# Kernel optimization log

Hardware: AMD Instinct MI355X
Metric: run time of the kernel (lower is better)

Reference implementation:

```python
import jax, jax.numpy as jnp
import numpy as np

D_MODEL = 1024
N_HEADS = 16
B, T = 16, 512


def setup_inputs() -> dict:
    key = jax.random.key(0)
    ks = jax.random.split(key, 5)
    s = 0.02
    return {
        "x": jax.random.normal(ks[0], (B, T, D_MODEL), dtype=jnp.float32),
        "w_qkv": jax.random.normal(ks[1], (D_MODEL, 3 * D_MODEL), dtype=jnp.float32) * s,
        "b_qkv": jax.random.normal(ks[2], (3 * D_MODEL,), dtype=jnp.float32) * s,
        "w_o": jax.random.normal(ks[3], (D_MODEL, D_MODEL), dtype=jnp.float32) * s,
        "b_o": jax.random.normal(ks[4], (D_MODEL,), dtype=jnp.float32) * s,
    }


def reference(x, w_qkv, b_qkv, w_o, b_o):
    Bx, Tx, C = x.shape
    H = N_HEADS
    hd = C // H
    qkv = x @ w_qkv + b_qkv                      # [B,T,3C]
    qkv = qkv.reshape(Bx, Tx, 3, H, hd).transpose(2, 0, 3, 1, 4)  # [3,B,H,T,hd]
    q, k, v = qkv[0], qkv[1], qkv[2]
    # NOTE: original scales by sqrt(C) = sqrt(d_model), not sqrt(head_dim)
    att = jnp.einsum("bhqd,bhkd->bhqk", q, k) / jnp.sqrt(jnp.float32(C))
    causal = jnp.tril(jnp.ones((Tx, Tx), dtype=bool))
    att = jnp.where(causal, att, -jnp.inf)
    att = jax.nn.softmax(att, axis=-1)
    y = jnp.einsum("bhqk,bhkd->bhqd", att, v)    # [B,H,T,hd]
    y = y.transpose(0, 2, 1, 3).reshape(Bx, Tx, C)
    return y @ w_o + b_o
```

## Files before the change

### kernel.cpp

```cpp
#include <hip/hip_runtime.h>
#include <cstddef>


#define B_  16
#define T_  512
#define C_  1024
#define H_  16
#define HD_ 64

typedef __bf16 bf16x8 __attribute__((ext_vector_type(8)));
typedef float  f32x4  __attribute__((ext_vector_type(4)));

__device__ __forceinline__ void gload16(const void* g, void* lds_dst) {
  __builtin_amdgcn_global_load_lds(
      (const __attribute__((address_space(1))) unsigned int*)g,
      (__attribute__((address_space(3))) unsigned int*)lds_dst, 16, 0, 0);
}

__global__ void cvt_kernel(const float* __restrict__ in, __bf16* __restrict__ out, int n) {
  int i = (blockIdx.x * 256 + threadIdx.x) * 8;
  if (i >= n) return;
  float4 f0 = *(const float4*)&in[i];
  float4 f1 = *(const float4*)&in[i + 4];
  bf16x8 o;
  o[0] = (__bf16)f0.x; o[1] = (__bf16)f0.y; o[2] = (__bf16)f0.z; o[3] = (__bf16)f0.w;
  o[4] = (__bf16)f1.x; o[5] = (__bf16)f1.y; o[6] = (__bf16)f1.z; o[7] = (__bf16)f1.w;
  *(bf16x8*)&out[i] = o;
}

__global__ void tconv_kernel(const float* __restrict__ w, __bf16* __restrict__ wt,
                             int K, int N) {
  __shared__ float tile[32][33];
  int tx = threadIdx.x, ty = threadIdx.y;
  int n0 = blockIdx.x * 32, k0 = blockIdx.y * 32;
  #pragma unroll
  for (int i = 0; i < 4; ++i) {
    int r = ty + i * 8;
    tile[r][tx] = w[(size_t)(k0 + r) * N + n0 + tx];
  }
  __syncthreads();
  #pragma unroll
  for (int i = 0; i < 4; ++i) {
    int r = ty + i * 8;
    wt[(size_t)(n0 + r) * K + k0 + tx] = (__bf16)tile[tx][r];
  }
}

__global__ void vtr_kernel(const __bf16* __restrict__ v, __bf16* __restrict__ vt) {
  __shared__ __bf16 tile[64][68];
  const int tid = threadIdx.x;
  const int bh = blockIdx.x, tc = blockIdx.y;
  const size_t base = (size_t)bh * T_ * HD_;
  #pragma unroll
  for (int p = 0; p < 2; ++p) {
    int t8 = p * 256 + tid;
    int r = t8 >> 3, col = (t8 & 7) * 8;
    *(bf16x8*)&tile[r][col] =
        *(const bf16x8*)&v[base + (size_t)(tc * 64 + r) * HD_ + col];
  }
  __syncthreads();
  #pragma unroll
  for (int p = 0; p < 2; ++p) {
    int t8 = p * 256 + tid;
    int d = t8 >> 3, tt = (t8 & 7) * 8;
    bf16x8 o;
    #pragma unroll
    for (int i = 0; i < 8; ++i) o[i] = tile[tt + i][d];
    *(bf16x8*)&vt[base + (size_t)d * T_ + tc * 64 + tt] = o;
  }
}

__global__ __launch_bounds__(512, 2) void gemm192_kernel(
    const __bf16* __restrict__ A, const __bf16* __restrict__ BT,
    const float* __restrict__ bias, int K, int NBn,
    __bf16* __restrict__ oq, __bf16* __restrict__ okk, __bf16* __restrict__ ov)
{
  extern __shared__ __align__(16) char lds[];
  const int tid = threadIdx.x, lane = tid & 63, wid = tid >> 6;
  const int wm = wid >> 2, wn = wid & 3;
  const int lr = lane & 15, lg = lane >> 4;

  const int cpx = gridDim.x >> 3;
  const int id = (blockIdx.x & 7) * cpx + (blockIdx.x >> 3);
  const int m0 = (id / NBn) * 256, n0 = (id % NBn) * 192;

  const int r8  = wid * 8 + (lane >> 3);
  const int csw = ((lane & 7) ^ (lane >> 3)) * 8;

  auto stageA = [&](const __bf16* g, char* dst) {
    #pragma unroll
    for (int i = 0; i < 4; ++i)
      gload16(g + (size_t)(i * 64 + r8) * K + csw, dst + i * 8192 + wid * 1024);
  };
  auto stageB = [&](const __bf16* g, char* dst) {
    #pragma unroll
    for (int i = 0; i < 3; ++i)
      gload16(g + (size_t)(i * 64 + r8) * K + csw, dst + i * 8192 + wid * 1024);
  };

  auto rdA = [&](bf16x8* d, const char* Ab) {
    #pragma unroll
    for (int mf = 0; mf < 8; ++mf) {
      const char* rp = Ab + (wm * 128 + mf * 16 + lr) * 128;
      #pragma unroll
      for (int ks = 0; ks < 2; ++ks)
        d[mf * 2 + ks] = *(const bf16x8*)(rp + (((ks << 2) + lg) ^ (lr & 7)) * 16);
    }
  };
  auto rdB = [&](bf16x8* d, const char* Bb) {
    #pragma unroll
    for (int nf = 0; nf < 3; ++nf) {
      const char* rp = Bb + (wn * 48 + nf * 16 + lr) * 128;
      #pragma unroll
      for (int ks = 0; ks < 2; ++ks)
        d[nf * 2 + ks] = *(const bf16x8*)(rp + (((ks << 2) + lg) ^ (lr & 7)) * 16);
    }
  };

  f32x4 acc[8][3] = {};

  auto mm = [&](int mh, const bf16x8* av, const bf16x8* bv) {
    __builtin_amdgcn_s_setprio(1);
    #pragma unroll
    for (int mf = 0; mf < 4; ++mf)
      #pragma unroll
      for (int nf = 0; nf < 3; ++nf)
        #pragma unroll
        for (int ks = 0; ks < 2; ++ks)
          acc[mh * 4 + mf][nf] = __builtin_amdgcn_mfma_f32_16x16x32_bf16(
              av[(mh * 4 + mf) * 2 + ks], bv[nf * 2 + ks], acc[mh * 4 + mf][nf],
              0, 0, 0);
    __builtin_amdgcn_s_setprio(0);
  };

  const int nt = K >> 6;
  const __bf16* gA = A  + (size_t)m0 * K;
  const __bf16* gB = BT + (size_t)n0 * K;
  char* const Ab0 = lds;
  char* const Bb0 = lds + 65536;

  stageA(gA, Ab0);
  stageB(gB, Bb0);
  stageA(gA + 64, Ab0 + 32768);

  bf16x8 a[16], b[6];

  for (int t = 0; t < nt; ++t) {
    const int p = t & 1;
    char* Ab = Ab0 + p * 32768;
    char* Bb = Bb0 + p * 24576;
    char* Bn = Bb0 + (p ^ 1) * 24576;

    if (t + 1 < nt) { asm volatile("s_waitcnt vmcnt(4)\ns_barrier" ::: "memory"); }
    else            { asm volatile("s_waitcnt vmcnt(0)\ns_barrier" ::: "memory"); }
    rdB(b, Bb);
    rdA(a, Ab);
    if (t + 1 < nt) stageB(gB + (size_t)(t + 1) * 64, Bn);
    mm(0, a, b);
    asm volatile("s_barrier" ::: "memory");

    if (t + 2 < nt) stageA(gA + (size_t)(t + 2) * 64, Ab);
    mm(1, a, b);
    asm volatile("s_barrier" ::: "memory");
  }

  #pragma unroll
  for (int nf = 0; nf < 3; ++nf) {
    int n = n0 + wn * 48 + nf * 16 + lr;
    float bv = bias[n];
    int which = n >> 10;
    __bf16* dst = (which == 0) ? oq : (which == 1) ? okk : ov;
    int h = (n >> 6) & 15, d = n & 63;
    #pragma unroll
    for (int mf = 0; mf < 8; ++mf)
      #pragma unroll
      for (int j = 0; j < 4; ++j) {
        int m = m0 + wm * 128 + mf * 16 + lg * 4 + j;
        int bb = m >> 9, tt = m & 511;
        dst[(size_t)((bb * H_ + h) * T_ + tt) * HD_ + d] =
            (__bf16)(acc[mf][nf][j] + bv);
      }
  }
}

__global__ __launch_bounds__(512, 2) void gemm128_kernel(
    const __bf16* __restrict__ A, const __bf16* __restrict__ BT,
    const float* __restrict__ bias, int K, int NBn, int N,
    float* __restrict__ out32)
{
  extern __shared__ __align__(16) char lds[];
  const int tid = threadIdx.x, lane = tid & 63, wid = tid >> 6;
  const int wm = wid >> 2, wn = wid & 3;
  const int lr = lane & 15, lg = lane >> 4;

  const int cpx = gridDim.x >> 3;
  const int id = (blockIdx.x & 7) * cpx + (blockIdx.x >> 3);
  const int m0 = (id / NBn) * 128, n0 = (id % NBn) * 256;

  const int r8  = wid * 8 + (lane >> 3);
  const int csw = ((lane & 7) ^ (lane >> 3)) * 8;

  auto stageA = [&](const __bf16* g, char* dst) {
    #pragma unroll
    for (int i = 0; i < 2; ++i)
      gload16(g + (size_t)(i * 64 + r8) * K + csw, dst + i * 8192 + wid * 1024);
  };
  auto stageB = [&](const __bf16* g, char* dst) {
    #pragma unroll
    for (int i = 0; i < 4; ++i)
      gload16(g + (size_t)(i * 64 + r8) * K + csw, dst + i * 8192 + wid * 1024);
  };

  auto rdA = [&](bf16x8* d, const char* Ab) {
    #pragma unroll
    for (int mf = 0; mf < 4; ++mf) {
      const char* rp = Ab + (wm * 64 + mf * 16 + lr) * 128;
      #pragma unroll
      for (int ks = 0; ks < 2; ++ks)
        d[mf * 2 + ks] = *(const bf16x8*)(rp + (((ks << 2) + lg) ^ (lr & 7)) * 16);
    }
  };
  auto rdB = [&](bf16x8* d, const char* Bb, int nh) {
    #pragma unroll
    for (int nfl = 0; nfl < 2; ++nfl) {
      const char* rp = Bb + (wn * 64 + (nh * 2 + nfl) * 16 + lr) * 128;
      #pragma unroll
      for (int ks = 0; ks < 2; ++ks)
        d[nfl * 2 + ks] = *(const bf16x8*)(rp + (((ks << 2) + lg) ^ (lr & 7)) * 16);
    }
  };

  f32x4 acc[4][4] = {};

  auto mm = [&](const bf16x8* av, const bf16x8* bv, int nh) {
    __builtin_amdgcn_s_setprio(1);
    #pragma unroll
    for (int mf = 0; mf < 4; ++mf)
      #pragma unroll
      for (int nfl = 0; nfl < 2; ++nfl)
        #pragma unroll
        for (int ks = 0; ks < 2; ++ks)
          acc[mf][nh * 2 + nfl] = __builtin_amdgcn_mfma_f32_16x16x32_bf16(
              av[mf * 2 + ks], bv[nfl * 2 + ks], acc[mf][nh * 2 + nfl], 0, 0, 0);
    __builtin_amdgcn_s_setprio(0);
  };

  const int nt = K >> 6;
  const __bf16* gA = A  + (size_t)m0 * K;
  const __bf16* gB = BT + (size_t)n0 * K;
  char* const Ab0 = lds;
  char* const Bb0 = lds + 32768;

  stageB(gB, Bb0);
  stageA(gA, Ab0);
  stageB(gB + 64, Bb0 + 32768);
  stageA(gA + 64, Ab0 + 16384);

  bf16x8 a[8], b0[4], b1[4];

  for (int t = 0; t < nt; ++t) {
    char* Ab = Ab0 + (t & 1) * 16384;
    char* Bb = Bb0 + (t % 3) * 32768;

    if (t + 1 < nt) { asm volatile("s_waitcnt vmcnt(6)\ns_barrier" ::: "memory"); }
    else            { asm volatile("s_waitcnt vmcnt(0)\ns_barrier" ::: "memory"); }
    rdA(a, Ab);
    rdB(b0, Bb, 0);
    if (t + 2 < nt) stageB(gB + (size_t)(t + 2) * 64, Bb0 + ((t + 2) % 3) * 32768);
    mm(a, b0, 0);
    asm volatile("s_barrier" ::: "memory");

    rdB(b1, Bb, 1);
    if (t + 2 < nt) stageA(gA + (size_t)(t + 2) * 64, Ab);
    mm(a, b1, 1);
    asm volatile("s_barrier" ::: "memory");
  }

  #pragma unroll
  for (int nf = 0; nf < 4; ++nf) {
    int n = n0 + wn * 64 + nf * 16 + lr;
    float bv = bias[n];
    #pragma unroll
    for (int mf = 0; mf < 4; ++mf)
      #pragma unroll
      for (int j = 0; j < 4; ++j) {
        int m = m0 + wm * 64 + mf * 16 + lg * 4 + j;
        out32[(size_t)m * N + n] = acc[mf][nf][j] + bv;
      }
  }
}

__global__ __launch_bounds__(256, 2) void attn_kernel(
    const __bf16* __restrict__ qb, const __bf16* __restrict__ kb,
    const __bf16* __restrict__ vtb, __bf16* __restrict__ y)
{
  __shared__ __attribute__((aligned(16))) __bf16 Ks[64][72];
  __shared__ __attribute__((aligned(16))) __bf16 Vt[64][72];
  __shared__ __attribute__((aligned(16))) __bf16 Ps[4][16][72];

  const int tid = threadIdx.x, lane = tid & 63, w = tid >> 6;
  const int lr = lane & 15, lg = lane >> 4;
  const int bh = blockIdx.x, qt = blockIdx.y;
  const size_t base = (size_t)bh * T_ * HD_;
  const int q0 = qt * 64 + w * 16;
  const float SCALE = 0.03125f;
  const float L2E = 1.44269504088896f;

  const int r_  = tid >> 3;
  const int c8_ = (tid & 7) * 8;

  bf16x8 qf[2];
  #pragma unroll
  for (int s = 0; s < 2; ++s)
    qf[s] = *(const bf16x8*)&qb[base + (size_t)(q0 + lr) * HD_ + s * 32 + lg * 8];

  f32x4 acc[4] = {};
  float mrun[4] = { -__builtin_inff(), -__builtin_inff(),
                    -__builtin_inff(), -__builtin_inff() };
  float lrun[4] = { 0.f, 0.f, 0.f, 0.f };

  bf16x8 kk[2], vv[2], kk2[2], vv2[2];
  #pragma unroll
  for (int p = 0; p < 2; ++p) {
    int rr = p * 32 + r_;
    kk[p] = *(const bf16x8*)&kb[base + (size_t)rr * HD_ + c8_];
    vv[p] = *(const bf16x8*)&vtb[base + (size_t)rr * T_ + c8_];
  }

  for (int c = 0; c <= qt; ++c) {
    #pragma unroll
    for (int p = 0; p < 2; ++p) {
      int rr = p * 32 + r_;
      *(bf16x8*)&Ks[rr][c8_] = kk[p];
      *(bf16x8*)&Vt[rr][c8_] = vv[p];
    }
    __syncthreads();

    if (c < qt) {
      #pragma unroll
      for (int p = 0; p < 2; ++p) {
        int rr = p * 32 + r_;
        kk2[p] = *(const bf16x8*)&kb[base + (size_t)(c + 1) * 64 * HD_ + (size_t)rr * HD_ + c8_];
        vv2[p] = *(const bf16x8*)&vtb[base + (size_t)rr * T_ + (c + 1) * 64 + c8_];
      }
    }

    f32x4 sc[4] = {};
    #pragma unroll
    for (int s = 0; s < 2; ++s) {
      #pragma unroll
      for (int cc = 0; cc < 4; ++cc) {
        bf16x8 kf = *(const bf16x8*)&Ks[cc * 16 + lr][s * 32 + lg * 8];
        sc[cc] = __builtin_amdgcn_mfma_f32_16x16x32_bf16(qf[s], kf, sc[cc], 0, 0, 0);
      }
    }

    #pragma unroll
    for (int cc = 0; cc < 4; ++cc)
      #pragma unroll
      for (int j = 0; j < 4; ++j) {
        float v = sc[cc][j] * SCALE;
        if (c == qt) {
          int kv = c * 64 + cc * 16 + lr;
          int qr = q0 + lg * 4 + j;
          if (kv > qr) v = -__builtin_inff();
        }
        sc[cc][j] = v;
      }

    float mx[4];
    #pragma unroll
    for (int j = 0; j < 4; ++j)
      mx[j] = fmaxf(fmaxf(sc[0][j], sc[1][j]), fmaxf(sc[2][j], sc[3][j]));
    #pragma unroll
    for (int msk = 1; msk <= 8; msk <<= 1)
      #pragma unroll
      for (int j = 0; j < 4; ++j)
        mx[j] = fmaxf(mx[j], __shfl_xor(mx[j], msk, 64));
    float corr[4];
    #pragma unroll
    for (int j = 0; j < 4; ++j) {
      float nm = fmaxf(mrun[j], mx[j]);
      corr[j] = exp2f((mrun[j] - nm) * L2E);
      mrun[j] = nm;
    }
    #pragma unroll
    for (int cc = 0; cc < 4; ++cc)
      #pragma unroll
      for (int j = 0; j < 4; ++j)
        sc[cc][j] = exp2f((sc[cc][j] - mrun[j]) * L2E);
    float rs[4];
    #pragma unroll
    for (int j = 0; j < 4; ++j)
      rs[j] = sc[0][j] + sc[1][j] + sc[2][j] + sc[3][j];
    #pragma unroll
    for (int msk = 1; msk <= 8; msk <<= 1)
      #pragma unroll
      for (int j = 0; j < 4; ++j)
        rs[j] += __shfl_xor(rs[j], msk, 64);
    #pragma unroll
    for (int j = 0; j < 4; ++j)
      lrun[j] = lrun[j] * corr[j] + rs[j];
    #pragma unroll
    for (int dd = 0; dd < 4; ++dd)
      #pragma unroll
      for (int j = 0; j < 4; ++j)
        acc[dd][j] *= corr[j];

    #pragma unroll
    for (int cc = 0; cc < 4; ++cc)
      #pragma unroll
      for (int j = 0; j < 4; ++j)
        Ps[w][lg * 4 + j][cc * 16 + lr] = (__bf16)sc[cc][j];

    #pragma unroll
    for (int s = 0; s < 2; ++s) {
      bf16x8 pa = *(const bf16x8*)&Ps[w][lr][s * 32 + lg * 8];
      #pragma unroll
      for (int dd = 0; dd < 4; ++dd) {
        bf16x8 vf = *(const bf16x8*)&Vt[dd * 16 + lr][s * 32 + lg * 8];
        acc[dd] = __builtin_amdgcn_mfma_f32_16x16x32_bf16(pa, vf, acc[dd], 0, 0, 0);
      }
    }
    __syncthreads();
    #pragma unroll
    for (int p = 0; p < 2; ++p) { kk[p] = kk2[p]; vv[p] = vv2[p]; }
  }

  const int b = bh >> 4, h = bh & 15;
  #pragma unroll
  for (int dd = 0; dd < 4; ++dd)
    #pragma unroll
    for (int j = 0; j < 4; ++j) {
      int t = q0 + lg * 4 + j;
      int d = dd * 16 + lr;
      y[((size_t)(b * T_ + t)) * C_ + h * HD_ + d] = (__bf16)(acc[dd][j] / lrun[j]);
    }
}

extern "C" void kernel_launch(void* const* d_in, const int* in_sizes, int n_in,
                              void* d_out, int out_size, void* d_ws, size_t ws_size,
                              hipStream_t stream) {
  const float* x    = (const float*)d_in[0];
  const float* wqkv = (const float*)d_in[1];
  const float* bqkv = (const float*)d_in[2];
  const float* wo   = (const float*)d_in[3];
  const float* bo   = (const float*)d_in[4];
  float* out = (float*)d_out;

  char* ws = (char*)d_ws;
  const size_t MB = 1u << 20;
  __bf16* xb    = (__bf16*)(ws);
  __bf16* wqt   = (__bf16*)(ws + 16 * MB);
  __bf16* wot   = (__bf16*)(ws + 22 * MB);
  __bf16* qbuf  = (__bf16*)(ws + 24 * MB);
  __bf16* kbuf  = (__bf16*)(ws + 40 * MB);
  __bf16* vbuf  = (__bf16*)(ws + 56 * MB);
  __bf16* ybuf  = (__bf16*)(ws + 56 * MB);
  __bf16* vtbuf = (__bf16*)(ws + 72 * MB);

  (void)hipFuncSetAttribute(reinterpret_cast<const void*>(&gemm192_kernel),
                            hipFuncAttributeMaxDynamicSharedMemorySize, 114688);
  (void)hipFuncSetAttribute(reinterpret_cast<const void*>(&gemm128_kernel),
                            hipFuncAttributeMaxDynamicSharedMemorySize, 131072);

  const int NX = B_ * T_ * C_;
  cvt_kernel<<<NX / (256 * 8), 256, 0, stream>>>(x, xb, NX);
  tconv_kernel<<<dim3(3 * C_ / 32, C_ / 32), dim3(32, 8), 0, stream>>>(wqkv, wqt, C_, 3 * C_);
  tconv_kernel<<<dim3(C_ / 32, C_ / 32), dim3(32, 8), 0, stream>>>(wo, wot, C_, C_);

  gemm192_kernel<<<512, 512, 114688, stream>>>(
      xb, wqt, bqkv, C_, 16, qbuf, kbuf, vbuf);

  vtr_kernel<<<dim3(B_ * H_, T_ / 64), 256, 0, stream>>>(vbuf, vtbuf);

  attn_kernel<<<dim3(B_ * H_, T_ / 64), 256, 0, stream>>>(qbuf, kbuf, vtbuf, ybuf);

  gemm128_kernel<<<256, 512, 131072, stream>>>(
      ybuf, wot, bo, C_, 4, C_, out);
}
```

Baseline: 149.8 us.

## Triple-buffer QKV GEMM loads in quarter phases and persist attention blocks over query tiles

The QKV GEMM moves to a three-stage A buffer and double-buffered B, and the K-step is split into four quarter phases. Each phase interleaves an LDS read, a slice of the next global-to-LDS stage and its MFMAs, separated by barriers, so loads overlap compute more finely. LDS per block grows to 144KB, which may lower occupancy below the two blocks per CU the launch bounds ask for. The attention kernel now launches 2 blocks per head instead of 8, and each block loops over alternating query tiles to balance the causal triangle. This cuts the block count and leaves fewer waves in flight, and the last prefetch of each tile now reloads chunk 0 for the next tile.

```diff
diff --git a/kernel.cpp b/kernel.cpp
--- a/kernel.cpp
+++ b/kernel.cpp
@@ -87,7 +87,14 @@
   const int r8  = wid * 8 + (lane >> 3);
   const int csw = ((lane & 7) ^ (lane >> 3)) * 8;
 
-  auto stageA = [&](const __bf16* g, char* dst) {
+  auto stageA2 = [&](const __bf16* g, char* dst, int half) {
+    #pragma unroll
+    for (int i = 0; i < 2; ++i) {
+      int ii = half * 2 + i;
+      gload16(g + (size_t)(ii * 64 + r8) * K + csw, dst + ii * 8192 + wid * 1024);
+    }
+  };
+  auto stageA4 = [&](const __bf16* g, char* dst) {
     #pragma unroll
     for (int i = 0; i < 4; ++i)
       gload16(g + (size_t)(i * 64 + r8) * K + csw, dst + i * 8192 + wid * 1024);
@@ -98,13 +105,13 @@
       gload16(g + (size_t)(i * 64 + r8) * K + csw, dst + i * 8192 + wid * 1024);
   };
 
-  auto rdA = [&](bf16x8* d, const char* Ab) {
-    #pragma unroll
-    for (int mf = 0; mf < 8; ++mf) {
-      const char* rp = Ab + (wm * 128 + mf * 16 + lr) * 128;
+  auto rdAg = [&](bf16x8* d, const char* Ab, int g) {
+    #pragma unroll
+    for (int mf2 = 0; mf2 < 2; ++mf2) {
+      const char* rp = Ab + (wm * 128 + (g * 2 + mf2) * 16 + lr) * 128;
       #pragma unroll
       for (int ks = 0; ks < 2; ++ks)
-        d[mf * 2 + ks] = *(const bf16x8*)(rp + (((ks << 2) + lg) ^ (lr & 7)) * 16);
+        d[mf2 * 2 + ks] = *(const bf16x8*)(rp + (((ks << 2) + lg) ^ (lr & 7)) * 16);
     }
   };
   auto rdB = [&](bf16x8* d, const char* Bb) {
@@ -119,50 +126,72 @@
 
   f32x4 acc[8][3] = {};
 
-  auto mm = [&](int mh, const bf16x8* av, const bf16x8* bv) {
+  auto mmg = [&](int g, const bf16x8* av, const bf16x8* bv) {
     __builtin_amdgcn_s_setprio(1);
     #pragma unroll
-    for (int mf = 0; mf < 4; ++mf)
+    for (int mf2 = 0; mf2 < 2; ++mf2)
       #pragma unroll
       for (int nf = 0; nf < 3; ++nf)
         #pragma unroll
         for (int ks = 0; ks < 2; ++ks)
-          acc[mh * 4 + mf][nf] = __builtin_amdgcn_mfma_f32_16x16x32_bf16(
-              av[(mh * 4 + mf) * 2 + ks], bv[nf * 2 + ks], acc[mh * 4 + mf][nf],
-              0, 0, 0);
+          acc[g * 2 + mf2][nf] = __builtin_amdgcn_mfma_f32_16x16x32_bf16(
+              av[mf2 * 2 + ks], bv[nf * 2 + ks], acc[g * 2 + mf2][nf], 0, 0, 0);
     __builtin_amdgcn_s_setprio(0);
   };
+
+#define MIDBAR() do { \
+    asm volatile("s_barrier\ns_waitcnt lgkmcnt(0)" ::: "memory"); \
+    __builtin_amdgcn_sched_barrier(0); } while (0)
+#define ENDBAR() asm volatile("s_barrier" ::: "memory")
 
   const int nt = K >> 6;
   const __bf16* gA = A  + (size_t)m0 * K;
   const __bf16* gB = BT + (size_t)n0 * K;
   char* const Ab0 = lds;
-  char* const Bb0 = lds + 65536;
-
-  stageA(gA, Ab0);
+  char* const Bb0 = lds + 98304;
+
+  stageA4(gA, Ab0);
   stageB(gB, Bb0);
-  stageA(gA + 64, Ab0 + 32768);
-
-  bf16x8 a[16], b[6];
+  stageA4(gA + 64, Ab0 + 32768);
+  stageB(gB + 64, Bb0 + 24576);
+  asm volatile("s_waitcnt vmcnt(7)\ns_barrier" ::: "memory");
+
+  bf16x8 a[4][4], b[6];
 
   for (int t = 0; t < nt; ++t) {
-    const int p = t & 1;
-    char* Ab = Ab0 + p * 32768;
-    char* Bb = Bb0 + p * 24576;
-    char* Bn = Bb0 + (p ^ 1) * 24576;
-
-    if (t + 1 < nt) { asm volatile("s_waitcnt vmcnt(4)\ns_barrier" ::: "memory"); }
-    else            { asm volatile("s_waitcnt vmcnt(0)\ns_barrier" ::: "memory"); }
+    const char* Ab = Ab0 + (t % 3) * 32768;
+    const char* Bb = Bb0 + (t & 1) * 24576;
+    char* Aw = Ab0 + ((t + 2) % 3) * 32768;
+    char* Bw = Bb0 + (t & 1) * 24576;
+    const bool st = (t + 2 < nt);
+
     rdB(b, Bb);
-    rdA(a, Ab);
-    if (t + 1 < nt) stageB(gB + (size_t)(t + 1) * 64, Bn);
-    mm(0, a, b);
-    asm volatile("s_barrier" ::: "memory");
-
-    if (t + 2 < nt) stageA(gA + (size_t)(t + 2) * 64, Ab);
-    mm(1, a, b);
-    asm volatile("s_barrier" ::: "memory");
-  }
+    rdAg(a[0], Ab, 0);
+    if (st) stageA2(gA + (size_t)(t + 2) * 64, Aw, 0);
+    MIDBAR();
+    mmg(0, a[0], b);
+    ENDBAR();
+
+    rdAg(a[1], Ab, 1);
+    if (st) stageA2(gA + (size_t)(t + 2) * 64, Aw, 1);
+    MIDBAR();
+    mmg(1, a[1], b);
+    ENDBAR();
+
+    rdAg(a[2], Ab, 2);
+    if (st) stageB(gB + (size_t)(t + 2) * 64, Bw);
+    MIDBAR();
+    mmg(2, a[2], b);
+    ENDBAR();
+
+    rdAg(a[3], Ab, 3);
+    MIDBAR();
+    mmg(3, a[3], b);
+    if (st) { asm volatile("s_waitcnt vmcnt(7)\ns_barrier" ::: "memory"); }
+    else    { asm volatile("s_waitcnt vmcnt(0)\ns_barrier" ::: "memory"); }
+  }
+#undef MIDBAR
+#undef ENDBAR
 
   #pragma unroll
   for (int nf = 0; nf < 3; ++nf) {
@@ -300,24 +329,14 @@
 
   const int tid = threadIdx.x, lane = tid & 63, w = tid >> 6;
   const int lr = lane & 15, lg = lane >> 4;
-  const int bh = blockIdx.x, qt = blockIdx.y;
+  const int bh = blockIdx.x, par = blockIdx.y;
   const size_t base = (size_t)bh * T_ * HD_;
-  const int q0 = qt * 64 + w * 16;
   const float SCALE = 0.03125f;
   const float L2E = 1.44269504088896f;
 
   const int r_  = tid >> 3;
   const int c8_ = (tid & 7) * 8;
-
-  bf16x8 qf[2];
-  #pragma unroll
-  for (int s = 0; s < 2; ++s)
-    qf[s] = *(const bf16x8*)&qb[base + (size_t)(q0 + lr) * HD_ + s * 32 + lg * 8];
-
-  f32x4 acc[4] = {};
-  float mrun[4] = { -__builtin_inff(), -__builtin_inff(),
-                    -__builtin_inff(), -__builtin_inff() };
-  float lrun[4] = { 0.f, 0.f, 0.f, 0.f };
+  const int b = bh >> 4, h = bh & 15;
 
   bf16x8 kk[2], vv[2], kk2[2], vv2[2];
   #pragma unroll
@@ -327,115 +346,129 @@
     vv[p] = *(const bf16x8*)&vtb[base + (size_t)rr * T_ + c8_];
   }
 
-  for (int c = 0; c <= qt; ++c) {
-    #pragma unroll
-    for (int p = 0; p < 2; ++p) {
-      int rr = p * 32 + r_;
-      *(bf16x8*)&Ks[rr][c8_] = kk[p];
-      *(bf16x8*)&Vt[rr][c8_] = vv[p];
-    }
-    __syncthreads();
-
-    if (c < qt) {
+  for (int qt = par; qt < 8; qt += 2) {
+    const int q0 = qt * 64 + w * 16;
+
+    bf16x8 qf[2];
+    #pragma unroll
+    for (int s = 0; s < 2; ++s)
+      qf[s] = *(const bf16x8*)&qb[base + (size_t)(q0 + lr) * HD_ + s * 32 + lg * 8];
+
+    f32x4 acc[4] = {};
+    float mrun[4] = { -__builtin_inff(), -__builtin_inff(),
+                      -__builtin_inff(), -__builtin_inff() };
+    float lrun[4] = { 0.f, 0.f, 0.f, 0.f };
+
+    for (int c = 0; c <= qt; ++c) {
       #pragma unroll
       for (int p = 0; p < 2; ++p) {
         int rr = p * 32 + r_;
-        kk2[p] = *(const bf16x8*)&kb[base + (size_t)(c + 1) * 64 * HD_ + (size_t)rr * HD_ + c8_];
-        vv2[p] = *(const bf16x8*)&vtb[base + (size_t)rr * T_ + (c + 1) * 64 + c8_];
-      }
+        *(bf16x8*)&Ks[rr][c8_] = kk[p];
+        *(bf16x8*)&Vt[rr][c8_] = vv[p];
+      }
+      __syncthreads();
+
+      {
+        int nc = (c < qt) ? c + 1 : 0;
+        #pragma unroll
+        for (int p = 0; p < 2; ++p) {
+          int rr = p * 32 + r_;
+          kk2[p] = *(const bf16x8*)&kb[base + (size_t)nc * 64 * HD_ + (size_t)rr * HD_ + c8_];
+          vv2[p] = *(const bf16x8*)&vtb[base + (size_t)rr * T_ + nc * 64 + c8_];
+        }
+      }
+
+      f32x4 sc[4] = {};
+      #pragma unroll
+      for (int s = 0; s < 2; ++s) {
+        #pragma unroll
+        for (int cc = 0; cc < 4; ++cc) {
+          bf16x8 kf = *(const bf16x8*)&Ks[cc * 16 + lr][s * 32 + lg * 8];
+          sc[cc] = __builtin_amdgcn_mfma_f32_16x16x32_bf16(qf[s], kf, sc[cc], 0, 0, 0);
+        }
+      }
+
+      #pragma unroll
+      for (int cc = 0; cc < 4; ++cc)
+        #pragma unroll
+        for (int j = 0; j < 4; ++j) {
+          float v = sc[cc][j] * SCALE;
+          if (c == qt) {
+            int kv = c * 64 + cc * 16 + lr;
+            int qr = q0 + lg * 4 + j;
+            if (kv > qr) v = -__builtin_inff();
+          }
+          sc[cc][j] = v;
+        }
+
+      float mx[4];
+      #pragma unroll
+      for (int j = 0; j < 4; ++j)
+        mx[j] = fmaxf(fmaxf(sc[0][j], sc[1][j]), fmaxf(sc[2][j], sc[3][j]));
+      #pragma unroll
+      for (int msk = 1; msk <= 8; msk <<= 1)
+        #pragma unroll
+        for (int j = 0; j < 4; ++j)
+          mx[j] = fmaxf(mx[j], __shfl_xor(mx[j], msk, 64));
+      float corr[4];
+      #pragma unroll
+      for (int j = 0; j < 4; ++j) {
+        float nm = fmaxf(mrun[j], mx[j]);
+        corr[j] = exp2f((mrun[j] - nm) * L2E);
+        mrun[j] = nm;
+      }
+      #pragma unroll
+      for (int cc = 0; cc < 4; ++cc)
+        #pragma unroll
+        for (int j = 0; j < 4; ++j)
+          sc[cc][j] = exp2f((sc[cc][j] - mrun[j]) * L2E);
+      float rs[4];
+      #pragma unroll
+      for (int j = 0; j < 4; ++j)
+        rs[j] = sc[0][j] + sc[1][j] + sc[2][j] + sc[3][j];
+      #pragma unroll
+      for (int msk = 1; msk <= 8; msk <<= 1)
+        #pragma unroll
+        for (int j = 0; j < 4; ++j)
+          rs[j] += __shfl_xor(rs[j], msk, 64);
+      #pragma unroll
+      for (int j = 0; j < 4; ++j)
+        lrun[j] = lrun[j] * corr[j] + rs[j];
+      #pragma unroll
+      for (int dd = 0; dd < 4; ++dd)
+        #pragma unroll
+        for (int j = 0; j < 4; ++j)
+          acc[dd][j] *= corr[j];
+
+      #pragma unroll
+      for (int cc = 0; cc < 4; ++cc)
+        #pragma unroll
+        for (int j = 0; j < 4; ++j)
+          Ps[w][lg * 4 + j][cc * 16 + lr] = (__bf16)sc[cc][j];
+
+      #pragma unroll
+      for (int s = 0; s < 2; ++s) {
+        bf16x8 pa = *(const bf16x8*)&Ps[w][lr][s * 32 + lg * 8];
+        #pragma unroll
+        for (int dd = 0; dd < 4; ++dd) {
+          bf16x8 vf = *(const bf16x8*)&Vt[dd * 16 + lr][s * 32 + lg * 8];
+          acc[dd] = __builtin_amdgcn_mfma_f32_16x16x32_bf16(pa, vf, acc[dd], 0, 0, 0);
+        }
+      }
+      __syncthreads();
+      #pragma unroll
+      for (int p = 0; p < 2; ++p) { kk[p] = kk2[p]; vv[p] = vv2[p]; }
     }
 
-    f32x4 sc[4] = {};
-    #pragma unroll
-    for (int s = 0; s < 2; ++s) {
-      #pragma unroll
-      for (int cc = 0; cc < 4; ++cc) {
-        bf16x8 kf = *(const bf16x8*)&Ks[cc * 16 + lr][s * 32 + lg * 8];
-        sc[cc] = __builtin_amdgcn_mfma_f32_16x16x32_bf16(qf[s], kf, sc[cc], 0, 0, 0);
-      }
-    }
-
-    #pragma unroll
-    for (int cc = 0; cc < 4; ++cc)
+    #pragma unroll
+    for (int dd = 0; dd < 4; ++dd)
       #pragma unroll
       for (int j = 0; j < 4; ++j) {
-        float v = sc[cc][j] * SCALE;
-        if (c == qt) {
-          int kv = c * 64 + cc * 16 + lr;
-          int qr = q0 + lg * 4 + j;
-          if (kv > qr) v = -__builtin_inff();
-        }
-        sc[cc][j] = v;
-      }
-
-    float mx[4];
-    #pragma unroll
-    for (int j = 0; j < 4; ++j)
-      mx[j] = fmaxf(fmaxf(sc[0][j], sc[1][j]), fmaxf(sc[2][j], sc[3][j]));
-    #pragma unroll
-    for (int msk = 1; msk <= 8; msk <<= 1)
-      #pragma unroll
-      for (int j = 0; j < 4; ++j)
-        mx[j] = fmaxf(mx[j], __shfl_xor(mx[j], msk, 64));
-    float corr[4];
-    #pragma unroll
-    for (int j = 0; j < 4; ++j) {
-      float nm = fmaxf(mrun[j], mx[j]);
-      corr[j] = exp2f((mrun[j] - nm) * L2E);
-      mrun[j] = nm;
-    }
-    #pragma unroll
-    for (int cc = 0; cc < 4; ++cc)
-      #pragma unroll
-      for (int j = 0; j < 4; ++j)
-        sc[cc][j] = exp2f((sc[cc][j] - mrun[j]) * L2E);
-    float rs[4];
-    #pragma unroll
-    for (int j = 0; j < 4; ++j)
-      rs[j] = sc[0][j] + sc[1][j] + sc[2][j] + sc[3][j];
-    #pragma unroll
-    for (int msk = 1; msk <= 8; msk <<= 1)
-      #pragma unroll
-      for (int j = 0; j < 4; ++j)
-        rs[j] += __shfl_xor(rs[j], msk, 64);
-    #pragma unroll
-    for (int j = 0; j < 4; ++j)
-      lrun[j] = lrun[j] * corr[j] + rs[j];
-    #pragma unroll
-    for (int dd = 0; dd < 4; ++dd)
-      #pragma unroll
-      for (int j = 0; j < 4; ++j)
-        acc[dd][j] *= corr[j];
-
-    #pragma unroll
-    for (int cc = 0; cc < 4; ++cc)
-      #pragma unroll
-      for (int j = 0; j < 4; ++j)
-        Ps[w][lg * 4 + j][cc * 16 + lr] = (__bf16)sc[cc][j];
-
-    #pragma unroll
-    for (int s = 0; s < 2; ++s) {
-      bf16x8 pa = *(const bf16x8*)&Ps[w][lr][s * 32 + lg * 8];
-      #pragma unroll
-      for (int dd = 0; dd < 4; ++dd) {
-        bf16x8 vf = *(const bf16x8*)&Vt[dd * 16 + lr][s * 32 + lg * 8];
-        acc[dd] = __builtin_amdgcn_mfma_f32_16x16x32_bf16(pa, vf, acc[dd], 0, 0, 0);
-      }
-    }
-    __syncthreads();
-    #pragma unroll
-    for (int p = 0; p < 2; ++p) { kk[p] = kk2[p]; vv[p] = vv2[p]; }
-  }
-
-  const int b = bh >> 4, h = bh & 15;
-  #pragma unroll
-  for (int dd = 0; dd < 4; ++dd)
-    #pragma unroll
-    for (int j = 0; j < 4; ++j) {
-      int t = q0 + lg * 4 + j;
-      int d = dd * 16 + lr;
-      y[((size_t)(b * T_ + t)) * C_ + h * HD_ + d] = (__bf16)(acc[dd][j] / lrun[j]);
-    }
+        int t = q0 + lg * 4 + j;
+        int d = dd * 16 + lr;
+        y[((size_t)(b * T_ + t)) * C_ + h * HD_ + d] = (__bf16)(acc[dd][j] / lrun[j]);
+      }
+  }
 }
 
 extern "C" void kernel_launch(void* const* d_in, const int* in_sizes, int n_in,
@@ -460,7 +493,7 @@
   __bf16* vtbuf = (__bf16*)(ws + 72 * MB);
 
   (void)hipFuncSetAttribute(reinterpret_cast<const void*>(&gemm192_kernel),
-                            hipFuncAttributeMaxDynamicSharedMemorySize, 114688);
+                            hipFuncAttributeMaxDynamicSharedMemorySize, 147456);
   (void)hipFuncSetAttribute(reinterpret_cast<const void*>(&gemm128_kernel),
                             hipFuncAttributeMaxDynamicSharedMemorySize, 131072);
 
@@ -469,12 +502,12 @@
   tconv_kernel<<<dim3(3 * C_ / 32, C_ / 32), dim3(32, 8), 0, stream>>>(wqkv, wqt, C_, 3 * C_);
   tconv_kernel<<<dim3(C_ / 32, C_ / 32), dim3(32, 8), 0, stream>>>(wo, wot, C_, C_);
 
-  gemm192_kernel<<<512, 512, 114688, stream>>>(
+  gemm192_kernel<<<512, 512, 147456, stream>>>(
       xb, wqt, bqkv, C_, 16, qbuf, kbuf, vbuf);
 
   vtr_kernel<<<dim3(B_ * H_, T_ / 64), 256, 0, stream>>>(vbuf, vtbuf);
 
-  attn_kernel<<<dim3(B_ * H_, T_ / 64), 256, 0, stream>>>(qbuf, kbuf, vtbuf, ybuf);
+  attn_kernel<<<dim3(B_ * H_, 2), 256, 0, stream>>>(qbuf, kbuf, vtbuf, ybuf);
 
   gemm128_kernel<<<256, 512, 131072, stream>>>(
       ybuf, wot, bo, C_, 4, C_, out);
```

New measurement: 156.5 us. +4.5%, slower.
